# Kernel tuning notes

Measured on AMD Instinct MI355X. Metric: run time of the kernel, lower is better.

The kernel has to match this reference:

```python
import jax, jax.numpy as jnp
import numpy as np

B, T, E, H = 8, 512, 64, 128
ALPHA, ETA, THETA = 0.999, 0.95, 0.05
BETA = 1.0 - ALPHA


def _l2norm_axis1(a):
    # torch F.normalize default: p=2, dim=1, eps=1e-12
    n = jnp.linalg.norm(a, axis=1, keepdims=True)
    return a / jnp.maximum(n, 1e-12)


def _mlp(W1, b1, W2, b2, x):
    # x: (B, E); per-batch-element MLP (ParallelMLPs)
    h = jax.nn.silu(jnp.einsum('bhe,be->bh', W1, x) + b1)  # (B, H)
    return jnp.einsum('beh,bh->be', W2, h) + b2            # (B, E)


def setup_inputs():
    key = jax.random.key(0)
    ks = jax.random.split(key, 5)
    x = jax.random.normal(ks[0], (B, T, E), jnp.float32)
    lim = float(np.sqrt(6.0 / (E + E)))  # xavier_uniform for K/V weights
    WK = jax.random.uniform(ks[1], (E, E), jnp.float32, -lim, lim)
    WV = jax.random.uniform(ks[2], (E, E), jnp.float32, -lim, lim)
    W1 = 0.02 * jax.random.normal(ks[3], (B, H, E), jnp.float32)  # template init std=0.02
    b1 = jnp.zeros((B, H), jnp.float32)
    W2 = 0.02 * jax.random.normal(ks[4], (B, E, H), jnp.float32)
    b2 = jnp.zeros((B, E), jnp.float32)
    SW1 = jnp.zeros((B, H, E), jnp.float32)
    Sb1 = jnp.zeros((B, H), jnp.float32)
    SW2 = jnp.zeros((B, E, H), jnp.float32)
    Sb2 = jnp.zeros((B, E), jnp.float32)
    return {"x": x, "WK": WK, "WV": WV, "W1": W1, "b1": b1, "W2": W2,
            "b2": b2, "SW1": SW1, "Sb1": Sb1, "SW2": SW2, "Sb2": Sb2}


def reference(x, WK, WV, W1, b1, W2, b2, SW1, Sb1, SW2, Sb2):
    # keys / values: Linear (no bias) -> SiLU -> L2-normalize along dim=1 (torch default)
    keys = _l2norm_axis1(jax.nn.silu(x @ WK.T))    # (B, T, E)
    values = _l2norm_axis1(jax.nn.silu(x @ WV.T))  # (B, T, E)
    kT = jnp.transpose(keys, (1, 0, 2))            # (T, B, E)
    vT = jnp.transpose(values, (1, 0, 2))

    def loss_fn(params, k, v):
        y = _mlp(*params, k)
        return jnp.mean((y - v) ** 2)

    # per-token grads & losses: vmap(grad_and_value) over the sequence dim
    losses, grads = jax.vmap(jax.value_and_grad(loss_fn), in_axes=(None, 0, 0))(
        (W1, b1, W2, b2), kT, vT)  # losses (T,), grads[i] (T, *param_shape)

    beta_vec = jnp.full((T,), BETA, jnp.float32)
    eta_vec = jnp.full((T,), ETA, jnp.float32)
    theta_vec = jnp.full((T,), THETA, jnp.float32)

    p_prefix = jnp.cumprod(beta_vec)
    p_suffix = jnp.cumprod(beta_vec[::-1])[::-1]
    q_prefix = jnp.cumprod(eta_vec)
    q_suffix = jnp.cumprod(eta_vec[::-1])[::-1]
    p_T = p_prefix[-1]
    q_T = q_prefix[-1]
    w = p_suffix / beta_vec * q_prefix
    A_T = w.sum()
    partial_sum = jnp.cumsum(w[::-1])[::-1]
    B_coeffs = -theta_vec * partial_sum / q_prefix
    D_coeffs = -theta_vec * q_suffix

    def upd(g, M0, S0):
        gB = jnp.tensordot(B_coeffs, g, axes=(0, 0))  # sum_t B[t] * g[t]
        gD = jnp.tensordot(D_coeffs, g, axes=(0, 0))
        return p_T * M0 + A_T * S0 + gB, q_T * S0 + gD

    new_state = [upd(g, M0, S0) for g, M0, S0 in
                 zip(grads, (W1, b1, W2, b2), (SW1, Sb1, SW2, Sb2))]
    parts = [losses] + [m.ravel() for m, _ in new_state] + [s.ravel() for _, s in new_state]
    return jnp.concatenate(parts)
```

## Files before the change

kernel.cpp:

```cpp
#include <hip/hip_runtime.h>
#include <math.h>

#define NB 8
#define NT 512
#define NE 64
#define NH 128

#define WS_K    0
#define WS_V    262144
#define WS_IVK  524288
#define WS_IVV  524800
#define WS_H    525312
#define WS_DY   1049600
#define WS_DZ   1311744
#define WS_LP   1836032

#define O_LOSS  0
#define O_MW1   512
#define O_MB1   66048
#define O_MW2   67072
#define O_MB2   132608
#define O_SW1   133120
#define O_SB1   198656
#define O_SW2   199680
#define O_SB2   265216

#define POISON_F (-3.0316488252093987e-13f)

__device__ __forceinline__ float bcast(float v, int lane) {
    return __uint_as_float(__builtin_amdgcn_readlane(__float_as_uint(v), (unsigned)lane));
}

__device__ __forceinline__ float silu_f(float x) {
    return x / (1.f + expf(-x));
}

__global__ __launch_bounds__(256) void k_kv(const float* __restrict__ x,
                                            const float* __restrict__ WK,
                                            const float* __restrict__ WV,
                                            float* __restrict__ ws) {
    __shared__ float sWK[64 * 65];
    __shared__ float sWV[64 * 65];
    __shared__ float rK[256], rV[256];
    int tid = threadIdx.x;
    for (int i = tid; i < 4096; i += 256) {
        int e = i >> 6, j = i & 63;
        sWK[e * 65 + j] = WK[i];
        sWV[e * 65 + j] = WV[i];
    }
    __syncthreads();
    int idx = blockIdx.x * 256 + tid;
    int row = idx >> 6, e = idx & 63;
    const float4* xr4 = (const float4*)(x + row * 64);
    float ak = 0.f, av = 0.f;
#pragma unroll
    for (int j4 = 0; j4 < 16; ++j4) {
        float4 xv = xr4[j4];
        const float* wk = &sWK[e * 65 + j4 * 4];
        const float* wv = &sWV[e * 65 + j4 * 4];
        ak += xv.x * wk[0] + xv.y * wk[1] + xv.z * wk[2] + xv.w * wk[3];
        av += xv.x * wv[0] + xv.y * wv[1] + xv.z * wv[2] + xv.w * wv[3];
    }
    float kk = silu_f(ak), vv = silu_f(av);
    ws[WS_K + idx] = kk;
    ws[WS_V + idx] = vv;
    rK[tid] = kk * kk;
    rV[tid] = vv * vv;
    __syncthreads();
    int b = blockIdx.x >> 7;
    if (tid < 64) {
        atomicAdd(&ws[WS_IVK + b * 64 + tid],
                  rK[tid] + rK[tid + 64] + rK[tid + 128] + rK[tid + 192]);
    } else if (tid < 128) {
        int l = tid & 63;
        atomicAdd(&ws[WS_IVV + b * 64 + l],
                  rV[l] + rV[l + 64] + rV[l + 128] + rV[l + 192]);
    }
}

__global__ __launch_bounds__(256) void k_fwdbwd(const float* __restrict__ W1,
                                               const float* __restrict__ b1,
                                               const float* __restrict__ W2,
                                               const float* __restrict__ b2,
                                               float* __restrict__ ws) {
    __shared__ float sW1[NE * NH];
    __shared__ float sW2[NE * NH];
    int tid = threadIdx.x;
    int b = blockIdx.x >> 6;
    int chunk = blockIdx.x & 63;
    int w = tid >> 6, l = tid & 63;

    const float4* W14 = (const float4*)(W1 + b * 8192);
    const float4* W24 = (const float4*)(W2 + b * 8192);
#pragma unroll
    for (int k4 = 0; k4 < 8; ++k4) {
        int i4 = tid + k4 * 256;
        float4 a = W14[i4];
        int i = i4 * 4;
        int hh = i >> 6, eb = i & 63;
        sW1[(eb + 0) * 128 + (hh ^ ((eb + 0) & 31))] = a.x;
        sW1[(eb + 1) * 128 + (hh ^ ((eb + 1) & 31))] = a.y;
        sW1[(eb + 2) * 128 + (hh ^ ((eb + 2) & 31))] = a.z;
        sW1[(eb + 3) * 128 + (hh ^ ((eb + 3) & 31))] = a.w;
        float4 c = W24[i4];
        int ee = i >> 7, hb = i & 127, sw = ee & 31;
        sW2[ee * 128 + ((hb + 0) ^ sw)] = c.x;
        sW2[ee * 128 + ((hb + 1) ^ sw)] = c.y;
        sW2[ee * 128 + ((hb + 2) ^ sw)] = c.z;
        sW2[ee * 128 + ((hb + 3) ^ sw)] = c.w;
    }
    __syncthreads();

    float ivK = 1.f / fmaxf(sqrtf(ws[WS_IVK + b * 64 + l] - POISON_F), 1e-12f);
    float ivV = 1.f / fmaxf(sqrtf(ws[WS_IVV + b * 64 + l] - POISON_F), 1e-12f);
    float b1lo = b1[b * 128 + l], b1hi = b1[b * 128 + 64 + l];
    float b2l = b2[b * 64 + l];
    int t0 = chunk * 8 + w * 2;

    int rowE[2], rowH[2];
    float kv[2], vv[2];
#pragma unroll
    for (int j = 0; j < 2; ++j) {
        int t = t0 + j;
        rowE[j] = (b * NT + t) * NE;
        rowH[j] = (b * NT + t) * NH;
        kv[j] = ws[WS_K + rowE[j] + l] * ivK;
        vv[j] = ws[WS_V + rowE[j] + l] * ivV;
    }

    float zlo[2], zhi[2];
#pragma unroll
    for (int j = 0; j < 2; ++j) { zlo[j] = b1lo; zhi[j] = b1hi; }
    for (int e = 0; e < 64; ++e) {
        int sw = e & 31;
        float w0 = sW1[e * 128 + (l ^ sw)];
        float w1 = sW1[e * 128 + (l ^ sw) + 64];
#pragma unroll
        for (int j = 0; j < 2; ++j) {
            float kk = bcast(kv[j], e);
            zlo[j] += w0 * kk;
            zhi[j] += w1 * kk;
        }
    }
    float hlo[2], hhi[2];
#pragma unroll
    for (int j = 0; j < 2; ++j) { hlo[j] = silu_f(zlo[j]); hhi[j] = silu_f(zhi[j]); }

    float y[2];
#pragma unroll
    for (int j = 0; j < 2; ++j) y[j] = b2l;
    {
        int sw2 = l & 31;
        for (int hh = 0; hh < 64; ++hh) {
            float w0 = sW2[l * 128 + (hh ^ sw2)];
            float w1 = sW2[l * 128 + (hh ^ sw2) + 64];
#pragma unroll
            for (int j = 0; j < 2; ++j) {
                y[j] += w0 * bcast(hlo[j], hh) + w1 * bcast(hhi[j], hh);
            }
        }
    }

    float dyv[2], lp[2];
#pragma unroll
    for (int j = 0; j < 2; ++j) {
        float d = y[j] - vv[j];
        dyv[j] = d * (2.f / 512.f);
        lp[j] = d * d;
    }
#pragma unroll
    for (int m = 32; m; m >>= 1) {
#pragma unroll
        for (int j = 0; j < 2; ++j) lp[j] += __shfl_xor(lp[j], m);
    }
    if (l == 0) {
#pragma unroll
        for (int j = 0; j < 2; ++j) ws[WS_LP + b * NT + t0 + j] = lp[j];
    }

    float dhlo[2] = {0.f, 0.f}, dhhi[2] = {0.f, 0.f};
    for (int e = 0; e < 64; ++e) {
        int sw = e & 31;
        float w0 = sW2[e * 128 + (l ^ sw)];
        float w1 = sW2[e * 128 + (l ^ sw) + 64];
#pragma unroll
        for (int j = 0; j < 2; ++j) {
            float dd = bcast(dyv[j], e);
            dhlo[j] += w0 * dd;
            dhhi[j] += w1 * dd;
        }
    }

#pragma unroll
    for (int j = 0; j < 2; ++j) {
        float slo = 1.f / (1.f + expf(-zlo[j]));
        float shi = 1.f / (1.f + expf(-zhi[j]));
        float dz0 = dhlo[j] * (slo * (1.f + zlo[j] * (1.f - slo)));
        float dz1 = dhhi[j] * (shi * (1.f + zhi[j] * (1.f - shi)));
        ws[WS_DZ + rowH[j] + l] = dz0;
        ws[WS_DZ + rowH[j] + 64 + l] = dz1;
        ws[WS_H + rowH[j] + l] = hlo[j];
        ws[WS_H + rowH[j] + 64 + l] = hhi[j];
        ws[WS_DY + rowE[j] + l] = dyv[j];
        ws[WS_K + rowE[j] + l] = kv[j];
    }
}

__global__ __launch_bounds__(1024) void k_state(const float* __restrict__ ws,
                                                const float* __restrict__ W1,
                                                const float* __restrict__ b1,
                                                const float* __restrict__ W2,
                                                const float* __restrict__ b2,
                                                const float* __restrict__ SW1,
                                                const float* __restrict__ Sb1,
                                                const float* __restrict__ SW2,
                                                const float* __restrict__ Sb2,
                                                float* __restrict__ out) {
    __shared__ float sBC[512], sDC[512], sSC[3];
    __shared__ float sM[1024], sS[1024], sMb[16], sSb[16];
    int bi = blockIdx.x, tid = threadIdx.x;

    if (bi == 512) {
        if (tid < 512) {
            float s = 0.f;
#pragma unroll
            for (int b = 0; b < NB; ++b) s += ws[WS_LP + b * NT + tid];
            out[O_LOSS + tid] = s * (1.f / 512.f);
        }
        return;
    }

    const float L2ETA = -0.07400058144f;
    const float L2R   = -9.89178369f;
    const float INV1MR = 1.0f / (1.0f - 0.001052631579f);
    if (tid < 512) {
        float ePow = exp2f((float)(511 - tid) * L2ETA);
        float rPow = exp2f((float)(512 - tid) * L2R);
        sBC[tid] = -0.05f * ePow * (1.f - rPow) * INV1MR;
        sDC[tid] = -0.05f * 0.95f * ePow;
    } else if (tid == 512) {
        float q = exp2f(512.f * L2ETA);
        sSC[0] = 0.f;
        sSC[1] = q * INV1MR;
        sSC[2] = q;
    }
    __syncthreads();

    int tg = tid >> 8;
    int t0 = tg * 128;
    float accM = 0.f, accS = 0.f, accMb = 0.f, accSb = 0.f;

    if (bi < 256) {
        int b = bi >> 5, hb = (bi & 31) << 2;
        int hidx = (tid >> 6) & 3, e = tid & 63;
        int h = hb + hidx;
        const float* kb = ws + WS_K + b * NT * NE + e;
        const float* dzb = ws + WS_DZ + b * NT * NH + h;
#pragma unroll 8
        for (int t = t0; t < t0 + 128; ++t) {
            float kvt = kb[t * NE];
            float dzt = dzb[t * NH];
            float gb = sBC[t] * dzt, gd = sDC[t] * dzt;
            accM += gb * kvt; accS += gd * kvt;
            accMb += gb;      accSb += gd;
        }
        sM[tid] = accM; sS[tid] = accS;
        if (e == 0) { sMb[tg * 4 + hidx] = accMb; sSb[tg * 4 + hidx] = accSb; }
        __syncthreads();
        float pT = sSC[0], AT = sSC[1], qT = sSC[2];
        if (tid < 256) {
            float m = sM[tid] + sM[tid + 256] + sM[tid + 512] + sM[tid + 768];
            float s = sS[tid] + sS[tid + 256] + sS[tid + 512] + sS[tid + 768];
            int idx = (b * NH + h) * NE + e;
            out[O_MW1 + idx] = pT * W1[idx] + AT * SW1[idx] + m;
            out[O_SW1 + idx] = qT * SW1[idx] + s;
        }
        if (tid < 4) {
            float mb = sMb[tid] + sMb[4 + tid] + sMb[8 + tid] + sMb[12 + tid];
            float sb = sSb[tid] + sSb[4 + tid] + sSb[8 + tid] + sSb[12 + tid];
            int ib = b * NH + hb + tid;
            out[O_MB1 + ib] = pT * b1[ib] + AT * Sb1[ib] + mb;
            out[O_SB1 + ib] = qT * Sb1[ib] + sb;
        }
    } else {
        int bi2 = bi - 256;
        int b = bi2 >> 5, eb = (bi2 & 31) << 1;
        int eidx = (tid >> 7) & 1, h = tid & 127;
        int e = eb + eidx;
        const float* dyb = ws + WS_DY + b * NT * NE + e;
        const float* hbuf = ws + WS_H + b * NT * NH + h;
#pragma unroll 8
        for (int t = t0; t < t0 + 128; ++t) {
            float dyt = dyb[t * NE];
            float hht = hbuf[t * NH];
            float gb = sBC[t] * dyt, gd = sDC[t] * dyt;
            accM += gb * hht; accS += gd * hht;
            accMb += gb;      accSb += gd;
        }
        sM[tid] = accM; sS[tid] = accS;
        if (h == 0) { sMb[tg * 4 + eidx] = accMb; sSb[tg * 4 + eidx] = accSb; }
        __syncthreads();
        float pT = sSC[0], AT = sSC[1], qT = sSC[2];
        if (tid < 256) {
            float m = sM[tid] + sM[tid + 256] + sM[tid + 512] + sM[tid + 768];
            float s = sS[tid] + sS[tid + 256] + sS[tid + 512] + sS[tid + 768];
            int idx = (b * NE + e) * NH + h;
            out[O_MW2 + idx] = pT * W2[idx] + AT * SW2[idx] + m;
            out[O_SW2 + idx] = qT * SW2[idx] + s;
        }
        if (tid < 2) {
            float mb = sMb[tid] + sMb[4 + tid] + sMb[8 + tid] + sMb[12 + tid];
            float sb = sSb[tid] + sSb[4 + tid] + sSb[8 + tid] + sSb[12 + tid];
            int ib = b * NE + eb + tid;
            out[O_MB2 + ib] = pT * b2[ib] + AT * Sb2[ib] + mb;
            out[O_SB2 + ib] = qT * Sb2[ib] + sb;
        }
    }
}

extern "C" void kernel_launch(void* const* d_in, const int* in_sizes, int n_in,
                              void* d_out, int out_size, void* d_ws, size_t ws_size,
                              hipStream_t stream) {
    const float* x   = (const float*)d_in[0];
    const float* WK  = (const float*)d_in[1];
    const float* WV  = (const float*)d_in[2];
    const float* W1  = (const float*)d_in[3];
    const float* b1  = (const float*)d_in[4];
    const float* W2  = (const float*)d_in[5];
    const float* b2  = (const float*)d_in[6];
    const float* SW1 = (const float*)d_in[7];
    const float* Sb1 = (const float*)d_in[8];
    const float* SW2 = (const float*)d_in[9];
    const float* Sb2 = (const float*)d_in[10];
    float* out = (float*)d_out;
    float* ws = (float*)d_ws;

    hipLaunchKernelGGL(k_kv,     dim3(1024), dim3(256),  0, stream, x, WK, WV, ws);
    hipLaunchKernelGGL(k_fwdbwd, dim3(512),  dim3(256),  0, stream, W1, b1, W2, b2, ws);
    hipLaunchKernelGGL(k_state,  dim3(513),  dim3(1024), 0, stream,
                       ws, W1, b1, W2, b2, SW1, Sb1, SW2, Sb2, out);
}
```

Measured before the change: 114.5 us.

## Fuse loss reduction into fwd/bwd kernel and drop normalized-key writeback

Accumulates the per-token loss directly into the output with atomics from the fwd/bwd kernel and zeroes it with a memset, removing the extra reduction block in the state kernel. It also stops writing the normalized keys back to workspace and instead applies the inverse key norm per feature inside the state kernel. The pT*W1/pT*W2 terms are dropped on the grounds that the decay product underflows to zero in fp32. This adds a memset launch and atomic contention on the loss entries, and makes the state kernel depend on the raw keys and norm buffers staying valid.

```diff
diff --git a/kernel.cpp b/kernel.cpp
--- a/kernel.cpp
+++ b/kernel.cpp
@@ -13,7 +13,6 @@
 #define WS_H    525312
 #define WS_DY   1049600
 #define WS_DZ   1311744
-#define WS_LP   1836032
 
 #define O_LOSS  0
 #define O_MW1   512
@@ -82,7 +81,8 @@
                                                const float* __restrict__ b1,
                                                const float* __restrict__ W2,
                                                const float* __restrict__ b2,
-                                               float* __restrict__ ws) {
+                                               float* __restrict__ ws,
+                                               float* __restrict__ out) {
     __shared__ float sW1[NE * NH];
     __shared__ float sW2[NE * NH];
     int tid = threadIdx.x;
@@ -175,7 +175,8 @@
     }
     if (l == 0) {
 #pragma unroll
-        for (int j = 0; j < 2; ++j) ws[WS_LP + b * NT + t0 + j] = lp[j];
+        for (int j = 0; j < 2; ++j)
+            atomicAdd(&out[O_LOSS + t0 + j], lp[j] * (1.f / 512.f));
     }
 
     float dhlo[2] = {0.f, 0.f}, dhhi[2] = {0.f, 0.f};
@@ -202,7 +203,6 @@
         ws[WS_H + rowH[j] + l] = hlo[j];
         ws[WS_H + rowH[j] + 64 + l] = hhi[j];
         ws[WS_DY + rowE[j] + l] = dyv[j];
-        ws[WS_K + rowE[j] + l] = kv[j];
     }
 }
 
@@ -216,19 +216,9 @@
                                                 const float* __restrict__ SW2,
                                                 const float* __restrict__ Sb2,
                                                 float* __restrict__ out) {
-    __shared__ float sBC[512], sDC[512], sSC[3];
+    __shared__ float sBC[512], sDC[512];
     __shared__ float sM[1024], sS[1024], sMb[16], sSb[16];
     int bi = blockIdx.x, tid = threadIdx.x;
-
-    if (bi == 512) {
-        if (tid < 512) {
-            float s = 0.f;
-#pragma unroll
-            for (int b = 0; b < NB; ++b) s += ws[WS_LP + b * NT + tid];
-            out[O_LOSS + tid] = s * (1.f / 512.f);
-        }
-        return;
-    }
 
     const float L2ETA = -0.07400058144f;
     const float L2R   = -9.89178369f;
@@ -238,13 +228,10 @@
         float rPow = exp2f((float)(512 - tid) * L2R);
         sBC[tid] = -0.05f * ePow * (1.f - rPow) * INV1MR;
         sDC[tid] = -0.05f * 0.95f * ePow;
-    } else if (tid == 512) {
-        float q = exp2f(512.f * L2ETA);
-        sSC[0] = 0.f;
-        sSC[1] = q * INV1MR;
-        sSC[2] = q;
     }
     __syncthreads();
+    float qT = exp2f(512.f * L2ETA);
+    float AT = qT * INV1MR;
 
     int tg = tid >> 8;
     int t0 = tg * 128;
@@ -254,6 +241,7 @@
         int b = bi >> 5, hb = (bi & 31) << 2;
         int hidx = (tid >> 6) & 3, e = tid & 63;
         int h = hb + hidx;
+        float ivK = 1.f / fmaxf(sqrtf(ws[WS_IVK + b * 64 + e] - POISON_F), 1e-12f);
         const float* kb = ws + WS_K + b * NT * NE + e;
         const float* dzb = ws + WS_DZ + b * NT * NH + h;
 #pragma unroll 8
@@ -264,22 +252,21 @@
             accM += gb * kvt; accS += gd * kvt;
             accMb += gb;      accSb += gd;
         }
-        sM[tid] = accM; sS[tid] = accS;
+        sM[tid] = accM * ivK; sS[tid] = accS * ivK;
         if (e == 0) { sMb[tg * 4 + hidx] = accMb; sSb[tg * 4 + hidx] = accSb; }
         __syncthreads();
-        float pT = sSC[0], AT = sSC[1], qT = sSC[2];
         if (tid < 256) {
             float m = sM[tid] + sM[tid + 256] + sM[tid + 512] + sM[tid + 768];
             float s = sS[tid] + sS[tid + 256] + sS[tid + 512] + sS[tid + 768];
             int idx = (b * NH + h) * NE + e;
-            out[O_MW1 + idx] = pT * W1[idx] + AT * SW1[idx] + m;
+            out[O_MW1 + idx] = AT * SW1[idx] + m;
             out[O_SW1 + idx] = qT * SW1[idx] + s;
         }
         if (tid < 4) {
             float mb = sMb[tid] + sMb[4 + tid] + sMb[8 + tid] + sMb[12 + tid];
             float sb = sSb[tid] + sSb[4 + tid] + sSb[8 + tid] + sSb[12 + tid];
             int ib = b * NH + hb + tid;
-            out[O_MB1 + ib] = pT * b1[ib] + AT * Sb1[ib] + mb;
+            out[O_MB1 + ib] = AT * Sb1[ib] + mb;
             out[O_SB1 + ib] = qT * Sb1[ib] + sb;
         }
     } else {
@@ -300,19 +287,18 @@
         sM[tid] = accM; sS[tid] = accS;
         if (h == 0) { sMb[tg * 4 + eidx] = accMb; sSb[tg * 4 + eidx] = accSb; }
         __syncthreads();
-        float pT = sSC[0], AT = sSC[1], qT = sSC[2];
         if (tid < 256) {
             float m = sM[tid] + sM[tid + 256] + sM[tid + 512] + sM[tid + 768];
             float s = sS[tid] + sS[tid + 256] + sS[tid + 512] + sS[tid + 768];
             int idx = (b * NE + e) * NH + h;
-            out[O_MW2 + idx] = pT * W2[idx] + AT * SW2[idx] + m;
+            out[O_MW2 + idx] = AT * SW2[idx] + m;
             out[O_SW2 + idx] = qT * SW2[idx] + s;
         }
         if (tid < 2) {
             float mb = sMb[tid] + sMb[4 + tid] + sMb[8 + tid] + sMb[12 + tid];
             float sb = sSb[tid] + sSb[4 + tid] + sSb[8 + tid] + sSb[12 + tid];
             int ib = b * NE + eb + tid;
-            out[O_MB2 + ib] = pT * b2[ib] + AT * Sb2[ib] + mb;
+            out[O_MB2 + ib] = AT * Sb2[ib] + mb;
             out[O_SB2 + ib] = qT * Sb2[ib] + sb;
         }
     }
@@ -335,8 +321,10 @@
     float* out = (float*)d_out;
     float* ws = (float*)d_ws;
 
+    hipMemsetAsync(out + O_LOSS, 0, 512 * sizeof(float), stream);
+
     hipLaunchKernelGGL(k_kv,     dim3(1024), dim3(256),  0, stream, x, WK, WV, ws);
-    hipLaunchKernelGGL(k_fwdbwd, dim3(512),  dim3(256),  0, stream, W1, b1, W2, b2, ws);
-    hipLaunchKernelGGL(k_state,  dim3(513),  dim3(1024), 0, stream,
+    hipLaunchKernelGGL(k_fwdbwd, dim3(512),  dim3(256),  0, stream, W1, b1, W2, b2, ws, out);
+    hipLaunchKernelGGL(k_state,  dim3(512),  dim3(1024), 0, stream,
                        ws, W1, b1, W2, b2, SW1, Sb1, SW2, Sb2, out);
 }
```

After: 119.4 us. 4.3% more time.
